# Kernel optimization log

Hardware: AMD Instinct MI355X
Metric: run time of the kernel (lower is better)

## Reference

```python
import jax, jax.numpy as jnp
import numpy as np

WIN = 7
SIZE = 56
HEADS = 16
DIM = 512
SHIFT = WIN // 2  # 3


def _rel_index():
    # Matches torch.meshgrid (ij) + flatten + pairwise diff indexing of the bias table.
    coords = np.stack(np.meshgrid(np.arange(WIN), np.arange(WIN), indexing='ij')).reshape(2, -1)  # [2,49]
    rel = (coords[:, :, None] - coords[:, None, :]).transpose(1, 2, 0)  # [49,49,2]
    rel[..., 0] += WIN - 1
    rel[..., 1] += WIN - 1
    rel[..., 0] *= 2 * WIN - 1
    return (rel[..., 0] + rel[..., 1]).reshape(-1)  # [49*49]


def _attn_mask():
    # Shifted-window mask: windows mixing different regions get -100 on cross pairs.
    img = np.zeros((SIZE, SIZE))
    sl = (slice(0, -WIN), slice(-WIN, -SHIFT), slice(-SHIFT, None))
    cnt = 0
    for h in sl:
        for w in sl:
            img[h, w] = cnt
            cnt += 1
    m = img.reshape(SIZE // WIN, WIN, SIZE // WIN, WIN).transpose(0, 2, 1, 3).reshape(-1, WIN * WIN)  # [nW,49]
    am = m[:, None, :] - m[:, :, None]  # [nW,49,49]
    return np.where(am != 0, -100.0, 0.0).astype(np.float32)


_REL_IDX = _rel_index()
_MASK = _attn_mask()  # [64,49,49]


def setup_inputs() -> dict:
    key = jax.random.key(0)
    ks = jax.random.split(key, 6)
    Bn, N, C = 2048, WIN * WIN, DIM
    return {
        'x': jax.random.normal(ks[0], (Bn, N, C), jnp.float32),
        'qkv_w': jax.random.normal(ks[1], (C, 3 * C), jnp.float32) * (C ** -0.5),
        'qkv_b': jax.random.normal(ks[2], (3 * C,), jnp.float32) * 0.02,
        'proj_w': jax.random.normal(ks[3], (C, C), jnp.float32) * (C ** -0.5),
        'proj_b': jax.random.normal(ks[4], (C,), jnp.float32) * 0.02,
        'bias_table': jax.random.normal(ks[5], ((2 * WIN - 1) ** 2, HEADS), jnp.float32) * 0.02,
    }


def reference(x, qkv_w, qkv_b, proj_w, proj_b, bias_table):
    Bn, N, C = x.shape
    D = C // HEADS
    qkv = (x @ qkv_w + qkv_b).reshape(Bn, N, 3, HEADS, D).transpose(2, 0, 3, 1, 4)  # [3,Bn,H,N,D]
    q, k, v = qkv[0] * (D ** -0.5), qkv[1], qkv[2]
    attn = jnp.einsum('bhnd,bhmd->bhnm', q, k)  # [Bn,H,N,N]
    bias = bias_table[jnp.asarray(_REL_IDX)].reshape(N, N, HEADS).transpose(2, 0, 1)  # [H,N,N]
    attn = attn + bias[None]
    mask = jnp.asarray(_MASK, x.dtype)  # [nW,N,N]
    nW = mask.shape[0]
    attn = attn.reshape(Bn // nW, nW, HEADS, N, N) + mask[None, :, None]
    attn = jax.nn.softmax(attn.reshape(Bn, HEADS, N, N), axis=-1)
    out = jnp.einsum('bhnm,bhmd->bhnd', attn, v).transpose(0, 2, 1, 3).reshape(Bn, N, C)
    return out @ proj_w + proj_b
```

## Files before the change

### kernel.cpp

```cpp
#include <hip/hip_runtime.h>
#include <hip/hip_bf16.h>
#include <stdint.h>


#define HEADS 16
#define NTOK  49
#define CH    512

typedef float  f32x4  __attribute__((ext_vector_type(4)));
typedef __bf16 bf16x8 __attribute__((ext_vector_type(8)));
typedef unsigned short u16;
typedef unsigned int   u32;

__device__ __forceinline__ u16 f2bf(float f) {
  return __builtin_bit_cast(u16, (__bf16)f);
}

__device__ __forceinline__ void gload16(const u16* g, u16* l) {
  __builtin_amdgcn_global_load_lds(
      (const __attribute__((address_space(1))) u32*)g,
      (__attribute__((address_space(3))) u32*)l, 16, 0, 0);
}

__global__ __launch_bounds__(256) void k_wprep(const float* __restrict__ qkv_w,
                                               const float* __restrict__ proj_w,
                                               const float* __restrict__ qkv_b,
                                               u16* __restrict__ Wt, u16* __restrict__ Pt,
                                               float* __restrict__ bias2) {
  const float sc = 0.17677669529663687f;
  int tid = blockIdx.x * 256 + threadIdx.x;
  const int T1 = 1536 * 512;
  if (tid < 1536) bias2[tid] = qkv_b[tid] * (tid < 512 ? sc : 1.f);
  if (tid < T1) {
    int n = tid >> 9, k = tid & 511;
    float v = qkv_w[k * 1536 + n];
    if (n < 512) v *= sc;
    Wt[tid] = f2bf(v);
  } else {
    int t2 = tid - T1;
    int n = t2 >> 9, k = t2 & 511;
    Pt[t2] = f2bf(proj_w[k * 512 + n]);
  }
}

__global__ __launch_bounds__(256) void k_xcast(const float* __restrict__ x,
                                               u16* __restrict__ xb) {
  int tid = blockIdx.x * 256 + threadIdx.x;
  const float4* xv = (const float4*)x;
  float4 a = xv[tid * 2], b = xv[tid * 2 + 1];
  u16 o[8] = {f2bf(a.x), f2bf(a.y), f2bf(a.z), f2bf(a.w),
              f2bf(b.x), f2bf(b.y), f2bf(b.z), f2bf(b.w)};
  ((int4*)xb)[tid] = *(const int4*)o;
}

__global__ __launch_bounds__(256) void k_tabs(const float* __restrict__ bias_table,
                                              float* __restrict__ biasM,
                                              float* __restrict__ maskT) {
  int tid = blockIdx.x * 256 + threadIdx.x;
  if (tid < 16 * 4096) {
    int h = tid >> 12, rc = tid & 4095, r = rc >> 6, c = rc & 63;
    float v = -1e30f;
    if (r < NTOK && c < NTOK) {
      int ih = r / 7, iw = r - ih * 7, jh = c / 7, jw = c - jh * 7;
      v = bias_table[((ih - jh + 6) * 13 + (iw - jw + 6)) * HEADS + h];
    }
    biasM[tid] = v;
  } else {
    int t2 = tid - 65536;
    int mw = t2 >> 12, rc = t2 & 4095, r = rc >> 6, c = rc & 63;
    float v = 0.f;
    if (r < NTOK && c < NTOK) {
      int mwR = (mw >> 3) * 7, mwC = (mw & 7) * 7;
      int ih = r / 7, iw = r - ih * 7, jh = c / 7, jw = c - jh * 7;
      int gih = mwR + ih, giw = mwC + iw, gjh = mwR + jh, gjw = mwC + jw;
      int ri = (gih < 49 ? 0 : (gih < 53 ? 1 : 2)) * 3 + (giw < 49 ? 0 : (giw < 53 ? 1 : 2));
      int rj = (gjh < 49 ? 0 : (gjh < 53 ? 1 : 2)) * 3 + (gjw < 49 ? 0 : (gjw < 53 ? 1 : 2));
      v = (ri != rj) ? -100.f : 0.f;
    }
    maskT[t2] = v;
  }
}

template<int OUT_F32>
__global__ __launch_bounds__(256) void k_gemm(const u16* __restrict__ A,
                                              const u16* __restrict__ Bt,
                                              const float* __restrict__ bias,
                                              void* __restrict__ Cp,
                                              int M, int Nn, int K, int nbn) {
  __shared__ u16 smem[2 * 16384];
  const int t   = threadIdx.x;
  const int q8  = gridDim.x >> 3;
  const int bid = (blockIdx.x & 7) * q8 + (blockIdx.x >> 3);
  const int cb  = bid % nbn, rb = bid / nbn;
  const int row0 = rb << 7, col0 = cb << 7;
  const int lane = t & 63, w = t >> 6;
  const int wr = (w >> 1) << 6, wc = (w & 1) << 6;
  const int lm = lane & 15, lk = lane >> 4;

  const f32x4 fz = {0.f, 0.f, 0.f, 0.f};
  f32x4 acc[4][4];
#pragma unroll
  for (int i = 0; i < 4; i++)
#pragma unroll
    for (int j = 0; j < 4; j++) acc[i][j] = fz;

  int gr[4], gc[4], gdb[4];
#pragma unroll
  for (int i = 0; i < 4; ++i) {
    int q = (i << 8) + t;
    gr[i]  = q >> 3;
    gc[i]  = (((q & 7) ^ (gr[i] & 7)) << 3);
    gdb[i] = ((i << 8) + (t & 192)) << 3;
  }
  int offA[4], offB[4];
#pragma unroll
  for (int i = 0; i < 4; ++i) {
    int rowA = wr + i * 16 + lm;
    offA[i] = rowA * 64 + ((lk ^ (rowA & 7)) << 3);
    int rowB = wc + i * 16 + lm;
    offB[i] = rowB * 64 + ((lk ^ (rowB & 7)) << 3);
  }

  auto stage = [&](int p, int kt) {
    const int kb = kt << 6;
    u16* dA = smem + p * 16384;
    u16* dB = dA + 8192;
#pragma unroll
    for (int i = 0; i < 4; ++i) {
      gload16(A  + (size_t)(row0 + gr[i]) * K + kb + gc[i], dA + gdb[i]);
      gload16(Bt + (size_t)(col0 + gr[i]) * K + kb + gc[i], dB + gdb[i]);
    }
  };

  const int nk = K >> 6;
  stage(0, 0);
  __syncthreads();
  int p = 0;
  for (int kt = 0; kt < nk; ++kt) {
    if (kt + 1 < nk) stage(p ^ 1, kt + 1);
    const u16* sA = smem + p * 16384;
    const u16* sB = sA + 8192;
    bf16x8 a[4][2], b[4][2];
#pragma unroll
    for (int mi = 0; mi < 4; ++mi) {
      a[mi][0] = *(const bf16x8*)(sA + offA[mi]);
      a[mi][1] = *(const bf16x8*)(sA + (offA[mi] ^ 32));
    }
#pragma unroll
    for (int ni = 0; ni < 4; ++ni) {
      b[ni][0] = *(const bf16x8*)(sB + offB[ni]);
      b[ni][1] = *(const bf16x8*)(sB + (offB[ni] ^ 32));
    }
#pragma unroll
    for (int kk = 0; kk < 2; ++kk)
#pragma unroll
      for (int mi = 0; mi < 4; ++mi)
#pragma unroll
        for (int ni = 0; ni < 4; ++ni)
          acc[mi][ni] = __builtin_amdgcn_mfma_f32_16x16x32_bf16(a[mi][kk], b[ni][kk],
                                                                acc[mi][ni], 0, 0, 0);
    __syncthreads();
    p ^= 1;
  }

  if constexpr (!OUT_F32) {
#pragma unroll
    for (int mi = 0; mi < 4; ++mi)
#pragma unroll
      for (int ni = 0; ni < 4; ++ni) {
        int col = wc + ni * 16 + lm;
        float bv = bias[col0 + col];
#pragma unroll
        for (int r = 0; r < 4; ++r)
          smem[(wr + mi * 16 + lk * 4 + r) * 136 + col] = f2bf(acc[mi][ni][r] + bv);
      }
    __syncthreads();
    const int rr = t >> 1, seg = t & 1;
    u16* dst = (u16*)Cp + (size_t)(row0 + rr) * Nn + col0 + seg * 64;
    const u16* src = smem + rr * 136 + seg * 64;
#pragma unroll
    for (int i = 0; i < 8; ++i)
      *(int4*)(dst + i * 8) = *(const int4*)(src + i * 8);
  } else {
    float* smf = (float*)smem;
    for (int half = 0; half < 2; ++half) {
      __syncthreads();
      if ((w >> 1) == half) {
#pragma unroll
        for (int mi = 0; mi < 4; ++mi)
#pragma unroll
          for (int ni = 0; ni < 4; ++ni) {
            int col = wc + ni * 16 + lm;
            float bv = bias[col0 + col];
#pragma unroll
            for (int r = 0; r < 4; ++r)
              smf[(mi * 16 + lk * 4 + r) * 132 + col] = acc[mi][ni][r] + bv;
          }
      }
      __syncthreads();
      const int rr = t >> 2, seg = t & 3;
      float* dst = (float*)Cp + (size_t)(row0 + half * 64 + rr) * Nn + col0 + seg * 32;
      const float* src = smf + rr * 132 + seg * 32;
#pragma unroll
      for (int i = 0; i < 8; ++i)
        *(float4*)(dst + i * 4) = *(const float4*)(src + i * 4);
    }
  }
}

__global__ __launch_bounds__(256) void k_attn(const u16* __restrict__ qkv,
                                              const float* __restrict__ biasM,
                                              const float* __restrict__ maskT,
                                              u16* __restrict__ aout) {
  __shared__ u16 sm[4 * 3264];
  const int wdx = blockIdx.x;
  const int mw  = wdx & 63;
  const int t   = threadIdx.x;
  const int wv  = t >> 6;
  const int l   = t & 63;
  const int lm  = l & 15, lk = l >> 4;
  const size_t tb = (size_t)wdx * NTOK;
  const u16* base = qkv + tb * 1536;
  u16* sV = sm + wv * 3264;
  u16* sP = sV + 2176;

  const int4  iz = make_int4(0, 0, 0, 0);
  const f32x4 fz = {0.f, 0.f, 0.f, 0.f};
  const float* mT = maskT + (mw << 12);

  for (int hh = 0; hh < 4; ++hh) {
    const int h = (wv << 2) + hh;

    {
      int4 vv[4] = {iz, iz, iz, iz};
      if (l < NTOK) {
        const u16* vp = base + (size_t)l * 1536 + 1024 + h * 32;
#pragma unroll
        for (int i = 0; i < 4; ++i) vv[i] = *(const int4*)(vp + i * 8);
      }
      const u16* u = (const u16*)vv;
#pragma unroll
      for (int d = 0; d < 32; ++d) sV[d * 68 + l] = u[d];
    }

    bf16x8 kf[4];
#pragma unroll
    for (int ni = 0; ni < 4; ++ni) {
      int krow = ni * 16 + lm;
      int4 ki = (krow < NTOK)
        ? *(const int4*)(base + (size_t)krow * 1536 + 512 + h * 32 + lk * 8) : iz;
      kf[ni] = __builtin_bit_cast(bf16x8, ki);
    }

    bf16x8 vb[2][2];
#pragma unroll
    for (int kt = 0; kt < 2; ++kt)
#pragma unroll
      for (int df = 0; df < 2; ++df)
        vb[kt][df] = *(const bf16x8*)(sV + (df * 16 + lm) * 68 + kt * 32 + lk * 8);

    const float* bM = biasM + (h << 12);

#pragma unroll
    for (int mi = 0; mi < 4; ++mi) {
      const int qrow = mi * 16 + lm;
      int4 qi = (qrow < NTOK)
        ? *(const int4*)(base + (size_t)qrow * 1536 + h * 32 + lk * 8) : iz;
      bf16x8 qf = __builtin_bit_cast(bf16x8, qi);

      f32x4 st[4];
#pragma unroll
      for (int ni = 0; ni < 4; ++ni) {
        const int o4 = (qrow << 6) + ni * 16 + lk * 4;
        float4 b4 = *(const float4*)(bM + o4);
        float4 m4 = *(const float4*)(mT + o4);
        f32x4 ci = {b4.x + m4.x, b4.y + m4.y, b4.z + m4.z, b4.w + m4.w};
        st[ni] = __builtin_amdgcn_mfma_f32_16x16x32_bf16(kf[ni], qf, ci, 0, 0, 0);
      }

      float mx = -3e38f;
#pragma unroll
      for (int ni = 0; ni < 4; ++ni)
#pragma unroll
        for (int r = 0; r < 4; ++r) mx = fmaxf(mx, st[ni][r]);
      mx = fmaxf(mx, __shfl_xor(mx, 16, 64));
      mx = fmaxf(mx, __shfl_xor(mx, 32, 64));
      float sum = 0.f;
#pragma unroll
      for (int ni = 0; ni < 4; ++ni)
#pragma unroll
        for (int r = 0; r < 4; ++r) {
          float p = __expf(st[ni][r] - mx);
          st[ni][r] = p;
          sum += p;
        }
      sum += __shfl_xor(sum, 16, 64);
      sum += __shfl_xor(sum, 32, 64);
      const float rinv = __builtin_amdgcn_rcpf(sum);

#pragma unroll
      for (int ni = 0; ni < 4; ++ni) {
        u16 pk[4] = {f2bf(st[ni][0] * rinv), f2bf(st[ni][1] * rinv),
                     f2bf(st[ni][2] * rinv), f2bf(st[ni][3] * rinv)};
        *(int2*)(sP + lm * 68 + ni * 16 + lk * 4) = *(const int2*)pk;
      }

      f32x4 o0 = fz, o1 = fz;
#pragma unroll
      for (int kt = 0; kt < 2; ++kt) {
        bf16x8 pa = *(const bf16x8*)(sP + lm * 68 + kt * 32 + lk * 8);
        o0 = __builtin_amdgcn_mfma_f32_16x16x32_bf16(pa, vb[kt][0], o0, 0, 0, 0);
        o1 = __builtin_amdgcn_mfma_f32_16x16x32_bf16(pa, vb[kt][1], o1, 0, 0, 0);
      }

#pragma unroll
      for (int r = 0; r < 4; ++r) {
        int tok = mi * 16 + lk * 4 + r;
        if (tok < NTOK) {
          size_t ob = (tb + tok) * CH + h * 32;
          aout[ob + lm]      = f2bf(o0[r]);
          aout[ob + 16 + lm] = f2bf(o1[r]);
        }
      }
    }
  }
}

extern "C" void kernel_launch(void* const* d_in, const int* in_sizes, int n_in,
                              void* d_out, int out_size, void* d_ws, size_t ws_size,
                              hipStream_t stream) {
  const float* x      = (const float*)d_in[0];
  const float* qkv_b  = (const float*)d_in[2];
  const float* proj_b = (const float*)d_in[4];
  const float* btab   = (const float*)d_in[5];

  char* ws   = (char*)d_ws;
  u16* Wt    = (u16*)ws;
  u16* Pt    = (u16*)(ws + 1572864);
  u16* qkv   = (u16*)(ws + 2097152);
  u16* aout  = (u16*)(ws + 2097152 + 308281344ull);
  u16* xb    = aout;
  float* biasM = (float*)(ws + 2097152 + 308281344ull + 102760448ull);
  float* maskT = biasM + 65536;
  float* bias2 = maskT + 262144;
  float* out = (float*)d_out;

  k_wprep<<<4096, 256, 0, stream>>>((const float*)d_in[1], (const float*)d_in[3],
                                    qkv_b, Wt, Pt, bias2);
  k_xcast<<<25088, 256, 0, stream>>>(x, xb);
  k_tabs<<<1280, 256, 0, stream>>>(btab, biasM, maskT);
  k_gemm<0><<<784 * 12, 256, 0, stream>>>(xb, Wt, bias2, (void*)qkv, 100352, 1536, 512, 12);
  k_attn<<<2048, 256, 0, stream>>>(qkv, biasM, maskT, aout);
  k_gemm<1><<<784 * 4, 256, 0, stream>>>(aout, Pt, proj_b, (void*)out, 100352, 512, 512, 4);
}
```

Baseline: 631.4 us.

## Enlarge GEMM tiles to 256x256 with 512 threads and finer-grained barriers

Both GEMMs move from 128x128 tiles with 4 waves to 256x256 tiles with 8 waves, each wave computing a 128x64 sub-tile (8x4 MFMA fragments). This raises arithmetic intensity per LDS byte and cuts global traffic per output. The main loop swaps __syncthreads for explicit vmcnt waits plus s_barrier so the next tile's async LDS loads can overlap compute. LDS grows to 128KB per block and accumulator registers double, which lowers occupancy, and the grid shrinks to fewer, larger blocks.

```diff
diff --git a/kernel.cpp b/kernel.cpp
--- a/kernel.cpp
+++ b/kernel.cpp
@@ -82,49 +82,52 @@
 }
 
 template<int OUT_F32>
-__global__ __launch_bounds__(256) void k_gemm(const u16* __restrict__ A,
-                                              const u16* __restrict__ Bt,
-                                              const float* __restrict__ bias,
-                                              void* __restrict__ Cp,
-                                              int M, int Nn, int K, int nbn) {
-  __shared__ u16 smem[2 * 16384];
+__global__ __launch_bounds__(512, 2) void k_gemm(const u16* __restrict__ A,
+                                                 const u16* __restrict__ Bt,
+                                                 const float* __restrict__ bias,
+                                                 void* __restrict__ Cp,
+                                                 int M, int Nn, int K, int nbn) {
+  __shared__ u16 smem[2 * 32768];
   const int t   = threadIdx.x;
   const int q8  = gridDim.x >> 3;
   const int bid = (blockIdx.x & 7) * q8 + (blockIdx.x >> 3);
   const int cb  = bid % nbn, rb = bid / nbn;
-  const int row0 = rb << 7, col0 = cb << 7;
+  const int row0 = rb << 8, col0 = cb << 8;
   const int lane = t & 63, w = t >> 6;
-  const int wr = (w >> 1) << 6, wc = (w & 1) << 6;
+  const int wr = (w >> 2) & 1, wc = w & 3;
   const int lm = lane & 15, lk = lane >> 4;
 
   const f32x4 fz = {0.f, 0.f, 0.f, 0.f};
-  f32x4 acc[4][4];
-#pragma unroll
-  for (int i = 0; i < 4; i++)
+  f32x4 acc[8][4];
+#pragma unroll
+  for (int i = 0; i < 8; i++)
 #pragma unroll
     for (int j = 0; j < 4; j++) acc[i][j] = fz;
 
   int gr[4], gc[4], gdb[4];
 #pragma unroll
   for (int i = 0; i < 4; ++i) {
-    int q = (i << 8) + t;
+    int q = (i << 9) + t;
     gr[i]  = q >> 3;
     gc[i]  = (((q & 7) ^ (gr[i] & 7)) << 3);
-    gdb[i] = ((i << 8) + (t & 192)) << 3;
-  }
-  int offA[4], offB[4];
+    gdb[i] = (i << 12) + ((t & 448) << 3);
+  }
+  int offA[8], offB[4];
+#pragma unroll
+  for (int i = 0; i < 8; ++i) {
+    int rowA = (wr << 7) + i * 16 + lm;
+    offA[i] = rowA * 64 + ((lk ^ (rowA & 7)) << 3);
+  }
 #pragma unroll
   for (int i = 0; i < 4; ++i) {
-    int rowA = wr + i * 16 + lm;
-    offA[i] = rowA * 64 + ((lk ^ (rowA & 7)) << 3);
-    int rowB = wc + i * 16 + lm;
+    int rowB = (wc << 6) + i * 16 + lm;
     offB[i] = rowB * 64 + ((lk ^ (rowB & 7)) << 3);
   }
 
   auto stage = [&](int p, int kt) {
     const int kb = kt << 6;
-    u16* dA = smem + p * 16384;
-    u16* dB = dA + 8192;
+    u16* dA = smem + p * 32768;
+    u16* dB = dA + 16384;
 #pragma unroll
     for (int i = 0; i < 4; ++i) {
       gload16(A  + (size_t)(row0 + gr[i]) * K + kb + gc[i], dA + gdb[i]);
@@ -134,73 +137,84 @@
 
   const int nk = K >> 6;
   stage(0, 0);
-  __syncthreads();
   int p = 0;
   for (int kt = 0; kt < nk; ++kt) {
-    if (kt + 1 < nk) stage(p ^ 1, kt + 1);
-    const u16* sA = smem + p * 16384;
-    const u16* sB = sA + 8192;
-    bf16x8 a[4][2], b[4][2];
-#pragma unroll
-    for (int mi = 0; mi < 4; ++mi) {
-      a[mi][0] = *(const bf16x8*)(sA + offA[mi]);
-      a[mi][1] = *(const bf16x8*)(sA + (offA[mi] ^ 32));
-    }
-#pragma unroll
-    for (int ni = 0; ni < 4; ++ni) {
-      b[ni][0] = *(const bf16x8*)(sB + offB[ni]);
-      b[ni][1] = *(const bf16x8*)(sB + (offB[ni] ^ 32));
-    }
-#pragma unroll
-    for (int kk = 0; kk < 2; ++kk)
-#pragma unroll
-      for (int mi = 0; mi < 4; ++mi)
+    if (kt + 1 < nk) {
+      stage(p ^ 1, kt + 1);
+      asm volatile("s_waitcnt vmcnt(8)" ::: "memory");
+    } else {
+      asm volatile("s_waitcnt vmcnt(0)" ::: "memory");
+    }
+    __builtin_amdgcn_s_barrier();
+    asm volatile("" ::: "memory");
+    const u16* sA = smem + p * 32768;
+    const u16* sB = sA + 16384;
+#pragma unroll
+    for (int kk = 0; kk < 2; ++kk) {
+      bf16x8 a[8], b[4];
+#pragma unroll
+      for (int mi = 0; mi < 8; ++mi)
+        a[mi] = *(const bf16x8*)(sA + (offA[mi] ^ (kk << 5)));
+#pragma unroll
+      for (int ni = 0; ni < 4; ++ni)
+        b[ni] = *(const bf16x8*)(sB + (offB[ni] ^ (kk << 5)));
+#pragma unroll
+      for (int mi = 0; mi < 8; ++mi)
 #pragma unroll
         for (int ni = 0; ni < 4; ++ni)
-          acc[mi][ni] = __builtin_amdgcn_mfma_f32_16x16x32_bf16(a[mi][kk], b[ni][kk],
+          acc[mi][ni] = __builtin_amdgcn_mfma_f32_16x16x32_bf16(a[mi], b[ni],
                                                                 acc[mi][ni], 0, 0, 0);
-    __syncthreads();
+    }
+    asm volatile("" ::: "memory");
+    __builtin_amdgcn_s_barrier();
+    asm volatile("" ::: "memory");
     p ^= 1;
   }
 
   if constexpr (!OUT_F32) {
-#pragma unroll
-    for (int mi = 0; mi < 4; ++mi)
-#pragma unroll
-      for (int ni = 0; ni < 4; ++ni) {
-        int col = wc + ni * 16 + lm;
-        float bv = bias[col0 + col];
-#pragma unroll
-        for (int r = 0; r < 4; ++r)
-          smem[(wr + mi * 16 + lk * 4 + r) * 136 + col] = f2bf(acc[mi][ni][r] + bv);
-      }
-    __syncthreads();
-    const int rr = t >> 1, seg = t & 1;
-    u16* dst = (u16*)Cp + (size_t)(row0 + rr) * Nn + col0 + seg * 64;
-    const u16* src = smem + rr * 136 + seg * 64;
-#pragma unroll
-    for (int i = 0; i < 8; ++i)
-      *(int4*)(dst + i * 8) = *(const int4*)(src + i * 8);
+    for (int half = 0; half < 2; ++half) {
+      __syncthreads();
+      if (wr == half) {
+#pragma unroll
+        for (int mi = 0; mi < 8; ++mi)
+#pragma unroll
+          for (int ni = 0; ni < 4; ++ni) {
+            int col = (wc << 6) + ni * 16 + lm;
+            float bv = bias[col0 + col];
+#pragma unroll
+            for (int r = 0; r < 4; ++r)
+              smem[(mi * 16 + lk * 4 + r) * 264 + col] = f2bf(acc[mi][ni][r] + bv);
+          }
+      }
+      __syncthreads();
+      const int row = t >> 2, seg = t & 3;
+      u16* dst = (u16*)Cp + (size_t)(row0 + half * 128 + row) * Nn + col0 + seg * 64;
+      const u16* src = smem + row * 264 + seg * 64;
+#pragma unroll
+      for (int i = 0; i < 8; ++i)
+        *(int4*)(dst + i * 8) = *(const int4*)(src + i * 8);
+    }
   } else {
     float* smf = (float*)smem;
-    for (int half = 0; half < 2; ++half) {
+    for (int q = 0; q < 4; ++q) {
       __syncthreads();
-      if ((w >> 1) == half) {
-#pragma unroll
-        for (int mi = 0; mi < 4; ++mi)
+      if (wr == (q >> 1)) {
+        const int mib = (q & 1) * 4;
+#pragma unroll
+        for (int mo = 0; mo < 4; ++mo)
 #pragma unroll
           for (int ni = 0; ni < 4; ++ni) {
-            int col = wc + ni * 16 + lm;
+            int col = (wc << 6) + ni * 16 + lm;
             float bv = bias[col0 + col];
 #pragma unroll
             for (int r = 0; r < 4; ++r)
-              smf[(mi * 16 + lk * 4 + r) * 132 + col] = acc[mi][ni][r] + bv;
+              smf[(mo * 16 + lk * 4 + r) * 264 + col] = acc[mib + mo][ni][r] + bv;
           }
       }
       __syncthreads();
-      const int rr = t >> 2, seg = t & 3;
-      float* dst = (float*)Cp + (size_t)(row0 + half * 64 + rr) * Nn + col0 + seg * 32;
-      const float* src = smf + rr * 132 + seg * 32;
+      const int row = t >> 3, seg = t & 7;
+      float* dst = (float*)Cp + (size_t)(row0 + q * 64 + row) * Nn + col0 + seg * 32;
+      const float* src = smf + row * 264 + seg * 32;
 #pragma unroll
       for (int i = 0; i < 8; ++i)
         *(float4*)(dst + i * 4) = *(const float4*)(src + i * 4);
@@ -349,7 +363,7 @@
                                     qkv_b, Wt, Pt, bias2);
   k_xcast<<<25088, 256, 0, stream>>>(x, xb);
   k_tabs<<<1280, 256, 0, stream>>>(btab, biasM, maskT);
-  k_gemm<0><<<784 * 12, 256, 0, stream>>>(xb, Wt, bias2, (void*)qkv, 100352, 1536, 512, 12);
+  k_gemm<0><<<392 * 6, 512, 0, stream>>>(xb, Wt, bias2, (void*)qkv, 100352, 1536, 512, 6);
   k_attn<<<2048, 256, 0, stream>>>(qkv, biasM, maskT, aout);
-  k_gemm<1><<<784 * 4, 256, 0, stream>>>(aout, Pt, proj_b, (void*)out, 100352, 512, 512, 4);
-}
+  k_gemm<1><<<392 * 2, 512, 0, stream>>>(aout, Pt, proj_b, (void*)out, 100352, 512, 512, 2);
+}
```

Result: slower. 657.9 us (+4.2%).
